# Kernel optimization log

Hardware: AMD Instinct MI355X
Metric: run time of the kernel (lower is better)

## Reference

```python
import jax, jax.numpy as jnp
import numpy as np

N, E, D_IN, HID, OUT, H = 20000, 320000, 128, 128, 128, 4

def _lin(key, fan_in, fan_out):
    kw, kb = jax.random.split(key)
    W = jax.random.normal(kw, (fan_in, fan_out), jnp.float32) * 0.05
    b = jax.random.normal(kb, (fan_out,), jnp.float32) * 0.05
    return W, b

def setup_inputs() -> dict:
    key = jax.random.key(0)
    ks = jax.random.split(key, 10)
    x = jax.random.normal(ks[0], (N, D_IN), jnp.float32)
    edge_index = jax.random.randint(ks[1], (2, E), 0, N, jnp.int32)
    # Layer 0: TransformerConv(D_IN -> HID, heads=H, concat=True)
    Wq0, bq0 = _lin(ks[2], D_IN, H * HID)
    Wk0, bk0 = _lin(ks[3], D_IN, H * HID)
    Wv0, bv0 = _lin(ks[4], D_IN, H * HID)
    Ws0, bs0 = _lin(ks[5], D_IN, H * HID)   # root/skip projection
    # Layer 1: TransformerConv(H*HID -> OUT, heads=H, concat=False)
    Wq1, bq1 = _lin(ks[6], H * HID, H * OUT)
    Wk1, bk1 = _lin(ks[7], H * HID, H * OUT)
    Wv1, bv1 = _lin(ks[8], H * HID, H * OUT)
    Ws1, bs1 = _lin(ks[9], H * HID, OUT)    # skip maps to OUT when concat=False
    return dict(x=x, edge_index=edge_index,
                Wq0=Wq0, bq0=bq0, Wk0=Wk0, bk0=bk0, Wv0=Wv0, bv0=bv0, Ws0=Ws0, bs0=bs0,
                Wq1=Wq1, bq1=bq1, Wk1=Wk1, bk1=bk1, Wv1=Wv1, bv1=bv1, Ws1=Ws1, bs1=bs1)

def _transformer_conv(x, src, dst, Wq, bq, Wk, bk, Wv, bv, Ws, bs, heads, out_ch, concat):
    n = x.shape[0]
    q = (x @ Wq + bq).reshape(n, heads, out_ch)
    k = (x @ Wk + bk).reshape(n, heads, out_ch)
    v = (x @ Wv + bv).reshape(n, heads, out_ch)
    # per-edge attention logits: [E, H]
    alpha = jnp.einsum('ehc,ehc->eh', q[dst], k[src]) / jnp.sqrt(jnp.float32(out_ch))
    # softmax grouped by destination node (numerically stable)
    m = jax.ops.segment_max(alpha, dst, num_segments=n)        # [N, H]
    alpha = jnp.exp(alpha - m[dst])
    s = jax.ops.segment_sum(alpha, dst, num_segments=n)       # [N, H]
    alpha = alpha / (s[dst] + 1e-16)
    # weighted scatter-add of messages: [N, H, C]
    out = jax.ops.segment_sum(alpha[..., None] * v[src], dst, num_segments=n)
    if concat:
        out = out.reshape(n, heads * out_ch)
    else:
        out = out.mean(axis=1)
    return out + x @ Ws + bs  # root weight (skip connection)

def reference(x, edge_index,
              Wq0, bq0, Wk0, bk0, Wv0, bv0, Ws0, bs0,
              Wq1, bq1, Wk1, bk1, Wv1, bv1, Ws1, bs1):
    src, dst = edge_index[0], edge_index[1]
    h = _transformer_conv(x, src, dst, Wq0, bq0, Wk0, bk0, Wv0, bv0, Ws0, bs0, H, HID, True)
    h = jax.nn.relu(h)  # dropout is identity in eval mode
    out = _transformer_conv(h, src, dst, Wq1, bq1, Wk1, bk1, Wv1, bv1, Ws1, bs1, H, OUT, False)
    return out
```

## Files before the change

kernel.cpp:

```cpp
#include <hip/hip_runtime.h>
#include <hip/hip_bf16.h>
#include <math.h>

#define HCH    512
#define OUTD   128
#define N0CAT  2048
#define N1CAT  1664
#define P0STR  1024
#define P1STR  640
#define KVW    1024

typedef __attribute__((ext_vector_type(8))) short short8v;
typedef __attribute__((ext_vector_type(8))) unsigned short ushort8v;
typedef __attribute__((ext_vector_type(4))) unsigned short ushort4v;
typedef __attribute__((ext_vector_type(4))) float floatx4;
typedef __attribute__((ext_vector_type(2))) float floatx2;
typedef __attribute__((ext_vector_type(2))) unsigned int uintx2;

__device__ inline float bf2f(unsigned short u) {
    return __uint_as_float(((unsigned)u) << 16);
}

__device__ inline unsigned short f2bf(float f) {
    return (unsigned short)__bfloat16_as_ushort(__float2bfloat16(f));
}

template <bool HI>
__device__ inline floatx2 fp8x2_to_f32(unsigned int w) {
    return __builtin_amdgcn_cvt_pk_f32_fp8(w, HI);
}

__device__ inline unsigned int f32x4_to_fp8(float a, float b, float c, float d) {
    int w = __builtin_amdgcn_cvt_pk_fp8_f32(a, b, 0, false);
    w = __builtin_amdgcn_cvt_pk_fp8_f32(c, d, w, true);
    return (unsigned int)w;
}

__device__ inline void gload_lds16(const void* g, void* l) {
    __builtin_amdgcn_global_load_lds(
        (const __attribute__((address_space(1))) unsigned int*)g,
        (__attribute__((address_space(3))) unsigned int*)l, 16, 0, 0);
}


__global__ void hist_kernel(const int* __restrict__ dst, int* __restrict__ deg, int E) {
    int e = blockIdx.x * 256 + threadIdx.x;
    if (e < E) atomicAdd(&deg[dst[e]], 1);
}

__global__ __launch_bounds__(1024) void scan_kernel(const int* __restrict__ deg,
                                                    int* __restrict__ indptr,
                                                    int* __restrict__ cursor, int n) {
    __shared__ int wavesum[16];
    __shared__ int carry_s;
    int t = threadIdx.x;
    int lane = t & 63;
    int w = t >> 6;
    if (t == 0) carry_s = 0;
    __syncthreads();
    for (int base = 0; base < n; base += 4096) {
        int idx = base + t * 4;
        int v0 = (idx + 0 < n) ? deg[idx + 0] : 0;
        int v1 = (idx + 1 < n) ? deg[idx + 1] : 0;
        int v2 = (idx + 2 < n) ? deg[idx + 2] : 0;
        int v3 = (idx + 3 < n) ? deg[idx + 3] : 0;
        int s1 = v0 + v1, s2 = s1 + v2, tot = s2 + v3;
        int x = tot;
        #pragma unroll
        for (int off = 1; off < 64; off <<= 1) {
            int y = __shfl_up(x, off);
            if (lane >= off) x += y;
        }
        if (lane == 63) wavesum[w] = x;
        __syncthreads();
        int woff = 0;
        for (int i = 0; i < w; i++) woff += wavesum[i];
        int carry = carry_s;
        int excl = carry + woff + x - tot;
        if (idx + 0 < n) { indptr[idx + 0] = excl;      cursor[idx + 0] = excl; }
        if (idx + 1 < n) { indptr[idx + 1] = excl + v0; cursor[idx + 1] = excl + v0; }
        if (idx + 2 < n) { indptr[idx + 2] = excl + s1; cursor[idx + 2] = excl + s1; }
        if (idx + 3 < n) { indptr[idx + 3] = excl + s2; cursor[idx + 3] = excl + s2; }
        __syncthreads();
        if (t == 0) {
            int s = 0;
            #pragma unroll
            for (int i = 0; i < 16; i++) s += wavesum[i];
            carry_s = carry + s;
        }
        __syncthreads();
    }
    if (t == 0) indptr[n] = carry_s;
}

__global__ void scatter_kernel(const int* __restrict__ src, const int* __restrict__ dst,
                               int* __restrict__ cursor, int* __restrict__ srcs_sorted, int E) {
    int e = blockIdx.x * 256 + threadIdx.x;
    if (e < E) {
        int d = dst[e];
        int pos = atomicAdd(&cursor[d], 1);
        srcs_sorted[pos] = src[e];
    }
}


__global__ void cast_bf16_kernel(const float* __restrict__ in, __hip_bfloat16* __restrict__ out, int n) {
    int i = blockIdx.x * 256 + threadIdx.x;
    if (i < n) out[i] = __float2bfloat16(in[i]);
}

__global__ __launch_bounds__(256) void tpose4_kernel(const float* __restrict__ W0,
                                                     const float* __restrict__ W1,
                                                     const float* __restrict__ W2,
                                                     const float* __restrict__ W3,
                                                     __hip_bfloat16* __restrict__ out,
                                                     int K, int C) {
    __shared__ float tile[32][33];
    int z = blockIdx.z;
    const float* W = (z == 0) ? W0 : (z == 1) ? W1 : (z == 2) ? W2 : W3;
    __hip_bfloat16* o = out + (size_t)z * C * K;
    int c0 = blockIdx.x * 32, k0 = blockIdx.y * 32;
    int tx = threadIdx.x & 31, ty = threadIdx.x >> 5;
    #pragma unroll
    for (int r = ty; r < 32; r += 8)
        tile[r][tx] = W[(size_t)(k0 + r) * C + c0 + tx];
    __syncthreads();
    #pragma unroll
    for (int r = ty; r < 32; r += 8)
        o[(size_t)(c0 + r) * K + k0 + tx] = __float2bfloat16(tile[tx][r]);
}

__global__ void biascat_kernel(const float* __restrict__ bq0, const float* __restrict__ bk0,
                               const float* __restrict__ bv0, const float* __restrict__ bs0,
                               const float* __restrict__ bq1, const float* __restrict__ bk1,
                               const float* __restrict__ bv1, const float* __restrict__ bs1,
                               float* __restrict__ bc0, float* __restrict__ bc1) {
    int i = blockIdx.x * 256 + threadIdx.x;
    if (i < N0CAT) {
        int sel = i >> 9, col = i & 511;
        const float* b = (sel == 0) ? bq0 : (sel == 1) ? bk0 : (sel == 2) ? bv0 : bs0;
        bc0[i] = b[col];
    }
    if (i < N1CAT) {
        if (i < 1536) {
            int sel = i >> 9, col = i & 511;
            const float* b = (sel == 0) ? bq1 : (sel == 1) ? bk1 : bv1;
            bc1[i] = b[col];
        } else {
            bc1[i] = bs1[i - 1536];
        }
    }
}


#define BM 128
#define BN 128
#define BK 64

__global__ __launch_bounds__(256) void gemm_mfma(const __hip_bfloat16* __restrict__ A,
                                                 const __hip_bfloat16* __restrict__ Bt,
                                                 const float* __restrict__ bias,
                                                 __hip_bfloat16* __restrict__ P,
                                                 int pstride,
                                                 unsigned char* __restrict__ KV8,
                                                 int M, int K, int Nd, int mt_pad) {
    __shared__ __hip_bfloat16 As[BM][BK];
    __shared__ __hip_bfloat16 Bs[BN][BK];
    int f = blockIdx.x;
    int mt = f % mt_pad, nt = f / mt_pad;
    int bm = mt * BM, bn = nt * BN;
    if (bm >= M) return;
    int t = threadIdx.x;
    int lane = t & 63, w = t >> 6;
    int quad = lane >> 4, l16 = lane & 15;
    int wm = (w >> 1) * 64, wn = (w & 1) * 64;

    int srow = w * 8 + (lane >> 3);
    int c8g = (lane & 7) ^ ((lane >> 3) & 7);
    const char* Ab = (const char*)(A + (size_t)(bm + srow) * K + c8g * 8);
    const char* Bb = (const char*)(Bt + (size_t)(bn + srow) * K + c8g * 8);
    char* Al = (char*)&As[0][0] + w * 1024;
    char* Bl = (char*)&Bs[0][0] + w * 1024;

    int sw = l16 & 7;

    floatx4 acc[4][4];
    #pragma unroll
    for (int i = 0; i < 4; i++)
        #pragma unroll
        for (int j = 0; j < 4; j++)
            acc[i][j] = (floatx4)0.0f;

    for (int k0 = 0; k0 < K; k0 += BK) {
        __syncthreads();
        #pragma unroll
        for (int i = 0; i < 4; i++) {
            size_t go = ((size_t)i * 32 * K + k0) * 2;
            gload_lds16(Ab + go, Al + i * 4096);
            gload_lds16(Bb + go, Bl + i * 4096);
        }
        __syncthreads();
        #pragma unroll
        for (int ks = 0; ks < BK; ks += 32) {
            int c8a = (quad + (ks >> 3)) ^ sw;
            short8v af[4], bfr[4];
            #pragma unroll
            for (int i = 0; i < 4; i++)
                af[i] = *(const short8v*)&As[wm + i * 16 + l16][c8a * 8];
            #pragma unroll
            for (int j = 0; j < 4; j++)
                bfr[j] = *(const short8v*)&Bs[wn + j * 16 + l16][c8a * 8];
            #pragma unroll
            for (int i = 0; i < 4; i++)
                #pragma unroll
                for (int j = 0; j < 4; j++)
                    acc[i][j] = __builtin_amdgcn_mfma_f32_16x16x32_bf16(bfr[j], af[i], acc[i][j], 0, 0, 0);
        }
    }

    #pragma unroll
    for (int i = 0; i < 4; i++) {
        int row = bm + wm + i * 16 + l16;
        if (row >= M) continue;
        #pragma unroll
        for (int j = 0; j < 4; j++) {
            int col = bn + wn + j * 16 + quad * 4;
            floatx4 bv = *(const floatx4*)(bias + col);
            float v0 = acc[i][j][0] + bv[0];
            float v1 = acc[i][j][1] + bv[1];
            float v2 = acc[i][j][2] + bv[2];
            float v3 = acc[i][j][3] + bv[3];
            if (col < 512) {
                ushort4v o = { f2bf(v0), f2bf(v1), f2bf(v2), f2bf(v3) };
                *(ushort4v*)(P + (size_t)row * pstride + col) = o;
            } else if (col < 1536) {
                *(unsigned int*)(KV8 + (size_t)row * KVW + (col - 512)) = f32x4_to_fp8(v0, v1, v2, v3);
            } else {
                ushort4v o = { f2bf(v0), f2bf(v1), f2bf(v2), f2bf(v3) };
                *(ushort4v*)(P + (size_t)row * pstride + 512 + (col - 1536)) = o;
            }
        }
    }
}


#define PF 4

__global__ __launch_bounds__(256) void attn_kernel(const __hip_bfloat16* __restrict__ P,
                                                   int pstride,
                                                   const unsigned char* __restrict__ KV8,
                                                   const int* __restrict__ indptr,
                                                   const int* __restrict__ srcs,
                                                   __hip_bfloat16* __restrict__ out_b,
                                                   float* __restrict__ out_f,
                                                   int n_nodes, int mode) {
    int wave = threadIdx.x >> 6;
    int lane = threadIdx.x & 63;
    int node = blockIdx.x * 4 + wave;
    if (node >= n_nodes) return;
    const float scale = 0.08838834764831845f;

    const __hip_bfloat16* Prow = P + (size_t)node * pstride;
    float qf[8];
    {
        ushort8v qu = *(const ushort8v*)(Prow + lane * 8);
        #pragma unroll
        for (int j = 0; j < 8; j++) qf[j] = bf2f(qu[j]) * scale;
    }

    float l = 0.f;
    float acc[8] = {0.f, 0.f, 0.f, 0.f, 0.f, 0.f, 0.f, 0.f};

    int e0 = indptr[node], e1 = indptr[node + 1];
    const unsigned char* Kb = KV8 + lane * 8;

    uintx2 kb[PF], vb[PF];
    #pragma unroll
    for (int i = 0; i < PF; i++) {
        if (e0 + i < e1) {
            int s = srcs[e0 + i];
            const unsigned char* kp = Kb + (size_t)s * KVW;
            kb[i] = *(const uintx2*)kp;
            vb[i] = *(const uintx2*)(kp + 512);
        }
    }

    int e = e0;
    for (; e + PF <= e1; e += PF) {
        #pragma unroll
        for (int i = 0; i < PF; i++) {
            uintx2 ku = kb[i];
            uintx2 vu = vb[i];
            int pe = e + i + PF;
            if (pe < e1) {
                int s = srcs[pe];
                const unsigned char* kp = Kb + (size_t)s * KVW;
                kb[i] = *(const uintx2*)kp;
                vb[i] = *(const uintx2*)(kp + 512);
            }
            floatx2 k01 = fp8x2_to_f32<false>(ku[0]);
            floatx2 k23 = fp8x2_to_f32<true >(ku[0]);
            floatx2 k45 = fp8x2_to_f32<false>(ku[1]);
            floatx2 k67 = fp8x2_to_f32<true >(ku[1]);
            float part = qf[0] * k01[0] + qf[1] * k01[1]
                       + qf[2] * k23[0] + qf[3] * k23[1]
                       + qf[4] * k45[0] + qf[5] * k45[1]
                       + qf[6] * k67[0] + qf[7] * k67[1];
            part += __shfl_xor(part, 1);
            part += __shfl_xor(part, 2);
            part += __shfl_xor(part, 4);
            part += __shfl_xor(part, 8);
            float p = __expf(part);
            l += p;
            floatx2 v01 = fp8x2_to_f32<false>(vu[0]);
            floatx2 v23 = fp8x2_to_f32<true >(vu[0]);
            floatx2 v45 = fp8x2_to_f32<false>(vu[1]);
            floatx2 v67 = fp8x2_to_f32<true >(vu[1]);
            acc[0] += p * v01[0];
            acc[1] += p * v01[1];
            acc[2] += p * v23[0];
            acc[3] += p * v23[1];
            acc[4] += p * v45[0];
            acc[5] += p * v45[1];
            acc[6] += p * v67[0];
            acc[7] += p * v67[1];
        }
    }
    #pragma unroll
    for (int i = 0; i < PF; i++) {
        if (e + i < e1) {
            uintx2 ku = kb[i];
            uintx2 vu = vb[i];
            floatx2 k01 = fp8x2_to_f32<false>(ku[0]);
            floatx2 k23 = fp8x2_to_f32<true >(ku[0]);
            floatx2 k45 = fp8x2_to_f32<false>(ku[1]);
            floatx2 k67 = fp8x2_to_f32<true >(ku[1]);
            float part = qf[0] * k01[0] + qf[1] * k01[1]
                       + qf[2] * k23[0] + qf[3] * k23[1]
                       + qf[4] * k45[0] + qf[5] * k45[1]
                       + qf[6] * k67[0] + qf[7] * k67[1];
            part += __shfl_xor(part, 1);
            part += __shfl_xor(part, 2);
            part += __shfl_xor(part, 4);
            part += __shfl_xor(part, 8);
            float p = __expf(part);
            l += p;
            floatx2 v01 = fp8x2_to_f32<false>(vu[0]);
            floatx2 v23 = fp8x2_to_f32<true >(vu[0]);
            floatx2 v45 = fp8x2_to_f32<false>(vu[1]);
            floatx2 v67 = fp8x2_to_f32<true >(vu[1]);
            acc[0] += p * v01[0];
            acc[1] += p * v01[1];
            acc[2] += p * v23[0];
            acc[3] += p * v23[1];
            acc[4] += p * v45[0];
            acc[5] += p * v45[1];
            acc[6] += p * v67[0];
            acc[7] += p * v67[1];
        }
    }
    float inv = (l > 0.f) ? 1.f / l : 0.f;

    if (mode == 0) {
        ushort8v su = *(const ushort8v*)(Prow + 512 + lane * 8);
        ushort8v o;
        #pragma unroll
        for (int j = 0; j < 8; j++) {
            float r = fmaxf(acc[j] * inv + bf2f(su[j]), 0.f);
            o[j] = f2bf(r);
        }
        *(ushort8v*)(out_b + (size_t)node * HCH + lane * 8) = o;
    } else {
        float r[8];
        #pragma unroll
        for (int j = 0; j < 8; j++) {
            r[j] = acc[j] * inv;
            r[j] += __shfl_xor(r[j], 16);
            r[j] += __shfl_xor(r[j], 32);
            r[j] *= 0.25f;
        }
        if (lane < 16) {
            const __hip_bfloat16* sp = Prow + 512 + lane * 8;
            float* op = out_f + (size_t)node * OUTD + lane * 8;
            #pragma unroll
            for (int j = 0; j < 8; j++) op[j] = r[j] + bf2f(__bfloat16_as_ushort(sp[j]));
        }
    }
}


static inline size_t align256(size_t x) { return (x + 255) & ~(size_t)255; }

extern "C" void kernel_launch(void* const* d_in, const int* in_sizes, int n_in,
                              void* d_out, int out_size, void* d_ws, size_t ws_size,
                              hipStream_t stream) {
    const float* x   = (const float*)d_in[0];
    const int*   ei  = (const int*)d_in[1];
    const float* Wq0 = (const float*)d_in[2];  const float* bq0 = (const float*)d_in[3];
    const float* Wk0 = (const float*)d_in[4];  const float* bk0 = (const float*)d_in[5];
    const float* Wv0 = (const float*)d_in[6];  const float* bv0 = (const float*)d_in[7];
    const float* Ws0 = (const float*)d_in[8];  const float* bs0 = (const float*)d_in[9];
    const float* Wq1 = (const float*)d_in[10]; const float* bq1 = (const float*)d_in[11];
    const float* Wk1 = (const float*)d_in[12]; const float* bk1 = (const float*)d_in[13];
    const float* Wv1 = (const float*)d_in[14]; const float* bv1 = (const float*)d_in[15];
    const float* Ws1 = (const float*)d_in[16]; const float* bs1 = (const float*)d_in[17];
    float* out = (float*)d_out;

    const int N = in_sizes[0] / 128;
    const int E = in_sizes[1] / 2;
    const int* src = ei;
    const int* dst = ei + E;

    int mtiles = (N + BM - 1) / BM;
    int mt_pad = (mtiles + 7) & ~7;
    const int Mpad = mt_pad * BM;

    char* ws = (char*)d_ws;
    __hip_bfloat16* P0  = (__hip_bfloat16*)ws; ws += align256((size_t)N * P0STR * 2);
    __hip_bfloat16* P1  = P0;
    __hip_bfloat16* Hbb = (__hip_bfloat16*)ws; ws += align256((size_t)Mpad * HCH * 2);
    __hip_bfloat16* Xb  = (__hip_bfloat16*)ws; ws += align256((size_t)Mpad * 128 * 2);
    unsigned char* KV8  = (unsigned char*)ws;  ws += align256((size_t)N * KVW);
    __hip_bfloat16* Wc0 = (__hip_bfloat16*)ws; ws += align256((size_t)N0CAT * 128 * 2);
    __hip_bfloat16* Wc1 = (__hip_bfloat16*)ws; ws += align256((size_t)N1CAT * 512 * 2);
    float* bc0 = (float*)ws; ws += align256((size_t)N0CAT * 4);
    float* bc1 = (float*)ws; ws += align256((size_t)N1CAT * 4);
    int* deg    = (int*)ws; ws += align256((size_t)N * 4);
    int* cursor = (int*)ws; ws += align256((size_t)N * 4);
    int* indptr = (int*)ws; ws += align256((size_t)(N + 2) * 4);
    int* srcs   = (int*)ws; ws += align256((size_t)E * 4);

    dim3 blk(256);

    (void)hipMemsetAsync(deg, 0, (size_t)N * 4, stream);
    hist_kernel<<<(E + 255) / 256, 256, 0, stream>>>(dst, deg, E);
    scan_kernel<<<1, 1024, 0, stream>>>(deg, indptr, cursor, N);
    scatter_kernel<<<(E + 255) / 256, 256, 0, stream>>>(src, dst, cursor, srcs, E);

    cast_bf16_kernel<<<((size_t)N * 128 + 255) / 256, blk, 0, stream>>>(x, Xb, N * 128);
    tpose4_kernel<<<dim3(512 / 32, 128 / 32, 4), blk, 0, stream>>>(Wq0, Wk0, Wv0, Ws0, Wc0, 128, 512);
    tpose4_kernel<<<dim3(512 / 32, 512 / 32, 3), blk, 0, stream>>>(Wq1, Wk1, Wv1, Wv1, Wc1, 512, 512);
    tpose4_kernel<<<dim3(128 / 32, 512 / 32, 1), blk, 0, stream>>>(Ws1, Ws1, Ws1, Ws1, Wc1 + (size_t)1536 * 512, 512, 128);
    biascat_kernel<<<(N0CAT + 255) / 256, blk, 0, stream>>>(bq0, bk0, bv0, bs0, bq1, bk1, bv1, bs1, bc0, bc1);

    gemm_mfma<<<dim3(mt_pad * (N0CAT / BN)), blk, 0, stream>>>(
        Xb, Wc0, bc0, P0, P0STR, KV8, N, 128, N0CAT, mt_pad);
    attn_kernel<<<(N + 3) / 4, blk, 0, stream>>>(P0, P0STR, KV8, indptr, srcs, Hbb, nullptr, N, 0);

    gemm_mfma<<<dim3(mt_pad * (N1CAT / BN)), blk, 0, stream>>>(
        Hbb, Wc1, bc1, P1, P1STR, KV8, N, 512, N1CAT, mt_pad);
    attn_kernel<<<(N + 3) / 4, blk, 0, stream>>>(P1, P1STR, KV8, indptr, srcs, nullptr, out, N, 1);
}
```

Before: 376.2 us.

## Load GEMM MFMA fragments directly from global memory instead of LDS staging

```diff
diff --git a/kernel.cpp b/kernel.cpp
--- a/kernel.cpp
+++ b/kernel.cpp
@@ -34,12 +34,6 @@
     int w = __builtin_amdgcn_cvt_pk_fp8_f32(a, b, 0, false);
     w = __builtin_amdgcn_cvt_pk_fp8_f32(c, d, w, true);
     return (unsigned int)w;
-}
-
-__device__ inline void gload_lds16(const void* g, void* l) {
-    __builtin_amdgcn_global_load_lds(
-        (const __attribute__((address_space(1))) unsigned int*)g,
-        (__attribute__((address_space(3))) unsigned int*)l, 16, 0, 0);
 }
 
 
@@ -164,8 +158,6 @@
                                                  int pstride,
                                                  unsigned char* __restrict__ KV8,
                                                  int M, int K, int Nd, int mt_pad) {
-    __shared__ __hip_bfloat16 As[BM][BK];
-    __shared__ __hip_bfloat16 Bs[BN][BK];
     int f = blockIdx.x;
     int mt = f % mt_pad, nt = f / mt_pad;
     int bm = mt * BM, bn = nt * BN;
@@ -175,14 +167,8 @@
     int quad = lane >> 4, l16 = lane & 15;
     int wm = (w >> 1) * 64, wn = (w & 1) * 64;
 
-    int srow = w * 8 + (lane >> 3);
-    int c8g = (lane & 7) ^ ((lane >> 3) & 7);
-    const char* Ab = (const char*)(A + (size_t)(bm + srow) * K + c8g * 8);
-    const char* Bb = (const char*)(Bt + (size_t)(bn + srow) * K + c8g * 8);
-    char* Al = (char*)&As[0][0] + w * 1024;
-    char* Bl = (char*)&Bs[0][0] + w * 1024;
-
-    int sw = l16 & 7;
+    const __hip_bfloat16* Ap = A + (size_t)(bm + wm + l16) * K + quad * 8;
+    const __hip_bfloat16* Bp = Bt + (size_t)(bn + wn + l16) * K + quad * 8;
 
     floatx4 acc[4][4];
     #pragma unroll
@@ -192,30 +178,26 @@
             acc[i][j] = (floatx4)0.0f;
 
     for (int k0 = 0; k0 < K; k0 += BK) {
-        __syncthreads();
+        short8v af[4][2], bfr[4][2];
         #pragma unroll
         for (int i = 0; i < 4; i++) {
-            size_t go = ((size_t)i * 32 * K + k0) * 2;
-            gload_lds16(Ab + go, Al + i * 4096);
-            gload_lds16(Bb + go, Bl + i * 4096);
-        }
-        __syncthreads();
-        #pragma unroll
-        for (int ks = 0; ks < BK; ks += 32) {
-            int c8a = (quad + (ks >> 3)) ^ sw;
-            short8v af[4], bfr[4];
-            #pragma unroll
-            for (int i = 0; i < 4; i++)
-                af[i] = *(const short8v*)&As[wm + i * 16 + l16][c8a * 8];
-            #pragma unroll
-            for (int j = 0; j < 4; j++)
-                bfr[j] = *(const short8v*)&Bs[wn + j * 16 + l16][c8a * 8];
+            const __hip_bfloat16* a = Ap + (size_t)i * 16 * K + k0;
+            af[i][0] = *(const short8v*)a;
+            af[i][1] = *(const short8v*)(a + 32);
+        }
+        #pragma unroll
+        for (int j = 0; j < 4; j++) {
+            const __hip_bfloat16* b = Bp + (size_t)j * 16 * K + k0;
+            bfr[j][0] = *(const short8v*)b;
+            bfr[j][1] = *(const short8v*)(b + 32);
+        }
+        #pragma unroll
+        for (int s = 0; s < 2; s++)
             #pragma unroll
             for (int i = 0; i < 4; i++)
                 #pragma unroll
                 for (int j = 0; j < 4; j++)
-                    acc[i][j] = __builtin_amdgcn_mfma_f32_16x16x32_bf16(bfr[j], af[i], acc[i][j], 0, 0, 0);
-        }
+                    acc[i][j] = __builtin_amdgcn_mfma_f32_16x16x32_bf16(bfr[j][s], af[i][s], acc[i][j], 0, 0, 0);
     }
 
     #pragma unroll
```

Result: slower. 492.2 us (+30.9%).
